# Performance work log

Hardware: AMD Instinct MI355X
Metric: run time of the kernel (lower is better)

## Reference

```python
import jax, jax.numpy as jnp
import numpy as np

N = 8192
IN_F = 256
OUT_F = 128
ALPHA = 0.2
NEG = -9000000000000000.0

def setup_inputs() -> dict:
    key = jax.random.key(0)
    k1, k2, k3, k4 = jax.random.split(key, 4)
    h = jax.random.normal(k1, (N, IN_F), dtype=jnp.float32)
    adj = jax.random.randint(k2, (N, N), 0, 2, dtype=jnp.int32)
    # xavier-uniform-like params
    limW = float(np.sqrt(6.0 / (IN_F + OUT_F)))
    W = jax.random.uniform(k3, (IN_F, OUT_F), minval=-limW, maxval=limW, dtype=jnp.float32)
    lima = float(np.sqrt(6.0 / (2 * OUT_F + 1)))
    a = jax.random.uniform(k4, (2 * OUT_F, 1), minval=-lima, maxval=lima, dtype=jnp.float32)
    return {"h": h, "adj": adj, "W": W, "a": a}

def reference(h, adj, W, a):
    Wh = h @ W  # [N, F]
    # e_ij = LeakyReLU(a1.Wh_i + a2.Wh_j) -- avoids [N,N,2F] intermediate
    a1 = a[:OUT_F, 0]  # [F]
    a2 = a[OUT_F:, 0]  # [F]
    f1 = Wh @ a1  # [N]
    f2 = Wh @ a2  # [N]
    e = jax.nn.leaky_relu(f1[:, None] + f2[None, :], negative_slope=ALPHA)  # [N,N]
    att = jnp.where(adj > 0, e, jnp.float32(NEG))
    att = jax.nn.softmax(att, axis=1)
    h_prime = att @ Wh  # [N, F]
    return h_prime
```

## Files before the change

kernel.cpp:

```cpp
#include <hip/hip_runtime.h>
#include <hip/hip_bf16.h>

#define N    8192
#define INF  256
#define OUTF 128
#define ALPHA 0.2f

typedef __attribute__((ext_vector_type(8))) short bf16x8;
typedef __attribute__((ext_vector_type(4))) float f32x4;

__device__ __forceinline__ unsigned short f2bf(float x) {
    union { float f; unsigned u; } v; v.f = x;
    unsigned r = v.u + 0x7fff + ((v.u >> 16) & 1);
    return (unsigned short)(r >> 16);
}
__device__ __forceinline__ float bf2f(unsigned short b) {
    union { unsigned u; float f; } v; v.u = ((unsigned)b) << 16;
    return v.f;
}

__global__ __launch_bounds__(256) void k1_wh(
        const float* __restrict__ h, const float* __restrict__ W,
        const float* __restrict__ a,
        unsigned short* __restrict__ WhTb, float* __restrict__ f1, float* __restrict__ f2) {
    __shared__ float hs[8][INF];
    const int t  = threadIdx.x;
    const int i0 = blockIdx.x * 8;

    #pragma unroll
    for (int u = 0; u < 2; ++u) {
        int idx = u * 256 + t;
        int r   = idx >> 6;
        int kq  = idx & 63;
        *(float4*)&hs[r][kq * 4] = *(const float4*)(h + (size_t)(i0 + r) * INF + kq * 4);
    }
    __syncthreads();

    const int rg = t >> 5;
    const int ct = t & 31;
    float acc[4] = {0.f, 0.f, 0.f, 0.f};

    #pragma unroll 8
    for (int k = 0; k < INF; ++k) {
        float4 wv = *(const float4*)(W + (size_t)k * OUTF + ct * 4);
        float  hx = hs[rg][k];
        acc[0] += hx * wv.x; acc[1] += hx * wv.y;
        acc[2] += hx * wv.z; acc[3] += hx * wv.w;
    }

    const int r0 = i0 + rg;
    const int jb = r0 >> 5;
    const int jo = r0 & 31;
    #pragma unroll
    for (int cc = 0; cc < 4; ++cc)
        WhTb[(size_t)jb * 4096 + (ct * 4 + cc) * 32 + jo] = f2bf(acc[cc]);

    const float4 a1v = *(const float4*)(a + ct * 4);
    const float4 a2v = *(const float4*)(a + OUTF + ct * 4);
    float p1 = acc[0]*a1v.x + acc[1]*a1v.y + acc[2]*a1v.z + acc[3]*a1v.w;
    float p2 = acc[0]*a2v.x + acc[1]*a2v.y + acc[2]*a2v.z + acc[3]*a2v.w;
    #pragma unroll
    for (int off = 16; off > 0; off >>= 1) {
        p1 += __shfl_down(p1, off, 32);
        p2 += __shfl_down(p2, off, 32);
    }
    if (ct == 0) { f1[r0] = p1; f2[r0] = p2; }
}

struct PF { int4 a0, a1; float4 g0, g1; };

__device__ __forceinline__ PF ldpf(const int* __restrict__ ap,
                                   const float* __restrict__ gp, int jt) {
    PF p;
    p.a0 = *(const int4*)  (ap + (size_t)jt * 32);
    p.a1 = *(const int4*)  (ap + (size_t)jt * 32 + 4);
    p.g0 = *(const float4*)(gp + (size_t)jt * 32);
    p.g1 = *(const float4*)(gp + (size_t)jt * 32 + 4);
    return p;
}

#define EXP1(AV, FV, IDX)                                                   \
    {                                                                       \
        float s_ = f1r + (FV);                                              \
        float e_ = s_ > 0.f ? s_ : ALPHA * s_;                              \
        float p_ = ((AV) > 0) ? __expf(e_) : 0.f;                           \
        unsigned short pb_ = f2bf(p_);                                      \
        afrag[IDX] = (short)pb_;                                            \
        dsum += bf2f(pb_);                                                  \
    }

#define K2ITER(PFV, JT)                                                     \
    {                                                                       \
        const unsigned short* wp_ = WhTb + ((size_t)(w * 32 + (JT))) * 4096 + laneb; \
        bf16x8 b0_ = *(const bf16x8*)(wp_);                                 \
        bf16x8 b1_ = *(const bf16x8*)(wp_ + 512);                           \
        bf16x8 b2_ = *(const bf16x8*)(wp_ + 1024);                          \
        bf16x8 b3_ = *(const bf16x8*)(wp_ + 1536);                          \
        bf16x8 b4_ = *(const bf16x8*)(wp_ + 2048);                          \
        bf16x8 b5_ = *(const bf16x8*)(wp_ + 2560);                          \
        bf16x8 b6_ = *(const bf16x8*)(wp_ + 3072);                          \
        bf16x8 b7_ = *(const bf16x8*)(wp_ + 3584);                          \
        int4 A0_ = PFV.a0, A1_ = PFV.a1;                                    \
        float4 F0_ = PFV.g0, F1_ = PFV.g1;                                  \
        if ((JT) + 2 < NT) PFV = ldpf(adjp, f2p, (JT) + 2);                 \
        bf16x8 afrag;                                                       \
        EXP1(A0_.x, F0_.x, 0) EXP1(A0_.y, F0_.y, 1)                         \
        EXP1(A0_.z, F0_.z, 2) EXP1(A0_.w, F0_.w, 3)                         \
        EXP1(A1_.x, F1_.x, 4) EXP1(A1_.y, F1_.y, 5)                         \
        EXP1(A1_.z, F1_.z, 6) EXP1(A1_.w, F1_.w, 7)                         \
        acc0 = __builtin_amdgcn_mfma_f32_16x16x32_bf16(afrag, b0_, acc0, 0, 0, 0); \
        acc1 = __builtin_amdgcn_mfma_f32_16x16x32_bf16(afrag, b1_, acc1, 0, 0, 0); \
        acc2 = __builtin_amdgcn_mfma_f32_16x16x32_bf16(afrag, b2_, acc2, 0, 0, 0); \
        acc3 = __builtin_amdgcn_mfma_f32_16x16x32_bf16(afrag, b3_, acc3, 0, 0, 0); \
        acc4 = __builtin_amdgcn_mfma_f32_16x16x32_bf16(afrag, b4_, acc4, 0, 0, 0); \
        acc5 = __builtin_amdgcn_mfma_f32_16x16x32_bf16(afrag, b5_, acc5, 0, 0, 0); \
        acc6 = __builtin_amdgcn_mfma_f32_16x16x32_bf16(afrag, b6_, acc6, 0, 0, 0); \
        acc7 = __builtin_amdgcn_mfma_f32_16x16x32_bf16(afrag, b7_, acc7, 0, 0, 0); \
    }

__global__ __launch_bounds__(512, 4) void k2_attn(
        const int* __restrict__ adj, const unsigned short* __restrict__ WhTb,
        const float* __restrict__ f1, const float* __restrict__ f2,
        float* __restrict__ out) {
    __shared__ float red[8][16][132];
    __shared__ float den_s[8][16];

    const int t    = threadIdx.x;
    const int w    = t >> 6;
    const int ln   = t & 63;
    const int m16  = ln & 15;
    const int quad = ln >> 4;
    const int i0   = blockIdx.x * 16;
    const int row  = i0 + m16;

    const float f1r = f1[row];
    const int   j0w = w * (N / 8);
    const int   NT  = (N / 8) / 32;

    const int*   adjp  = adj + (size_t)row * N + j0w + quad * 8;
    const float* f2p   = f2 + j0w + quad * 8;
    const int    laneb = m16 * 32 + quad * 8;

    f32x4 acc0 = {0.f,0.f,0.f,0.f}, acc1 = {0.f,0.f,0.f,0.f};
    f32x4 acc2 = {0.f,0.f,0.f,0.f}, acc3 = {0.f,0.f,0.f,0.f};
    f32x4 acc4 = {0.f,0.f,0.f,0.f}, acc5 = {0.f,0.f,0.f,0.f};
    f32x4 acc6 = {0.f,0.f,0.f,0.f}, acc7 = {0.f,0.f,0.f,0.f};
    float dsum = 0.f;

    PF pf0 = ldpf(adjp, f2p, 0);
    PF pf1 = ldpf(adjp, f2p, 1);

    for (int jt = 0; jt < NT; jt += 2) {
        K2ITER(pf0, jt)
        K2ITER(pf1, jt + 1)
    }

    dsum += __shfl_xor(dsum, 16);
    dsum += __shfl_xor(dsum, 32);
    if (quad == 0) den_s[w][m16] = dsum;

    #pragma unroll
    for (int r = 0; r < 4; ++r) {
        red[w][quad * 4 + r][0 * 16 + m16] = acc0[r];
        red[w][quad * 4 + r][1 * 16 + m16] = acc1[r];
        red[w][quad * 4 + r][2 * 16 + m16] = acc2[r];
        red[w][quad * 4 + r][3 * 16 + m16] = acc3[r];
        red[w][quad * 4 + r][4 * 16 + m16] = acc4[r];
        red[w][quad * 4 + r][5 * 16 + m16] = acc5[r];
        red[w][quad * 4 + r][6 * 16 + m16] = acc6[r];
        red[w][quad * 4 + r][7 * 16 + m16] = acc7[r];
    }
    __syncthreads();

    {
        int r  = t >> 5;
        int c4 = (t & 31) * 4;
        float4 sv = {0.f,0.f,0.f,0.f};
        float dtot = 0.f;
        #pragma unroll
        for (int ww = 0; ww < 8; ++ww) {
            float4 v = *(const float4*)&red[ww][r][c4];
            sv.x += v.x; sv.y += v.y; sv.z += v.z; sv.w += v.w;
            dtot += den_s[ww][r];
        }
        const float inv = 1.0f / dtot;
        float4 o = {sv.x * inv, sv.y * inv, sv.z * inv, sv.w * inv};
        *(float4*)(out + (size_t)(i0 + r) * OUTF + c4) = o;
    }
}

extern "C" void kernel_launch(void* const* d_in, const int* in_sizes, int n_in,
                              void* d_out, int out_size, void* d_ws, size_t ws_size,
                              hipStream_t stream) {
    const float* h   = (const float*)d_in[0];
    const int*   adj = (const int*)  d_in[1];
    const float* W   = (const float*)d_in[2];
    const float* a   = (const float*)d_in[3];
    float* out = (float*)d_out;

    unsigned short* WhTb = (unsigned short*)d_ws;
    float* f1 = (float*)(WhTb + (size_t)N * OUTF);
    float* f2 = f1 + N;

    k1_wh  <<<N / 8, 256, 0, stream>>>(h, W, a, WhTb, f1, f2);
    k2_attn<<<N / 16, 512, 0, stream>>>(adj, WhTb, f1, f2, out);
}
```

Before: 527.9 us.

## Split attention K-range over 4 waves and load f2 on demand

Reduces the attention kernel block from 8 waves to 4, so each wave covers twice as many columns and the cross-wave shared-memory reduction is half the size. Only the adjacency ints stay in the two-deep register prefetch; f2 values are now loaded inline in each step, which cuts register pressure. Launch bounds change from (512,4) to (256,3). The adj read stays the dominant traffic, so the main risks are fewer waves in flight to hide HBM latency and exposed f2 load latency.

```diff
diff --git a/kernel.cpp b/kernel.cpp
--- a/kernel.cpp
+++ b/kernel.cpp
@@ -67,15 +67,12 @@
     if (ct == 0) { f1[r0] = p1; f2[r0] = p2; }
 }
 
-struct PF { int4 a0, a1; float4 g0, g1; };
-
-__device__ __forceinline__ PF ldpf(const int* __restrict__ ap,
-                                   const float* __restrict__ gp, int jt) {
-    PF p;
-    p.a0 = *(const int4*)  (ap + (size_t)jt * 32);
-    p.a1 = *(const int4*)  (ap + (size_t)jt * 32 + 4);
-    p.g0 = *(const float4*)(gp + (size_t)jt * 32);
-    p.g1 = *(const float4*)(gp + (size_t)jt * 32 + 4);
+struct PFA { int4 a0, a1; };
+
+__device__ __forceinline__ PFA ldadj(const int* __restrict__ ap, int jt) {
+    PFA p;
+    p.a0 = *(const int4*)(ap + (size_t)jt * 32);
+    p.a1 = *(const int4*)(ap + (size_t)jt * 32 + 4);
     return p;
 }
 
@@ -89,9 +86,9 @@
         dsum += bf2f(pb_);                                                  \
     }
 
-#define K2ITER(PFV, JT)                                                     \
+#define K2STEP(PFV, JT)                                                     \
     {                                                                       \
-        const unsigned short* wp_ = WhTb + ((size_t)(w * 32 + (JT))) * 4096 + laneb; \
+        const unsigned short* wp_ = WhTb + ((size_t)(w * 64 + (JT))) * 4096 + laneb; \
         bf16x8 b0_ = *(const bf16x8*)(wp_);                                 \
         bf16x8 b1_ = *(const bf16x8*)(wp_ + 512);                           \
         bf16x8 b2_ = *(const bf16x8*)(wp_ + 1024);                          \
@@ -100,9 +97,10 @@
         bf16x8 b5_ = *(const bf16x8*)(wp_ + 2560);                          \
         bf16x8 b6_ = *(const bf16x8*)(wp_ + 3072);                          \
         bf16x8 b7_ = *(const bf16x8*)(wp_ + 3584);                          \
+        float4 F0_ = *(const float4*)(f2p + (size_t)(JT) * 32);             \
+        float4 F1_ = *(const float4*)(f2p + (size_t)(JT) * 32 + 4);         \
         int4 A0_ = PFV.a0, A1_ = PFV.a1;                                    \
-        float4 F0_ = PFV.g0, F1_ = PFV.g1;                                  \
-        if ((JT) + 2 < NT) PFV = ldpf(adjp, f2p, (JT) + 2);                 \
+        if ((JT) + 2 < NT) PFV = ldadj(adjp, (JT) + 2);                     \
         bf16x8 afrag;                                                       \
         EXP1(A0_.x, F0_.x, 0) EXP1(A0_.y, F0_.y, 1)                         \
         EXP1(A0_.z, F0_.z, 2) EXP1(A0_.w, F0_.w, 3)                         \
@@ -118,12 +116,12 @@
         acc7 = __builtin_amdgcn_mfma_f32_16x16x32_bf16(afrag, b7_, acc7, 0, 0, 0); \
     }
 
-__global__ __launch_bounds__(512, 4) void k2_attn(
+__global__ __launch_bounds__(256, 3) void k2_attn(
         const int* __restrict__ adj, const unsigned short* __restrict__ WhTb,
         const float* __restrict__ f1, const float* __restrict__ f2,
         float* __restrict__ out) {
-    __shared__ float red[8][16][132];
-    __shared__ float den_s[8][16];
+    __shared__ float red[4][16][132];
+    __shared__ float den_s[4][16];
 
     const int t    = threadIdx.x;
     const int w    = t >> 6;
@@ -134,8 +132,8 @@
     const int row  = i0 + m16;
 
     const float f1r = f1[row];
-    const int   j0w = w * (N / 8);
-    const int   NT  = (N / 8) / 32;
+    const int   j0w = w * (N / 4);
+    const int   NT  = (N / 4) / 32;
 
     const int*   adjp  = adj + (size_t)row * N + j0w + quad * 8;
     const float* f2p   = f2 + j0w + quad * 8;
@@ -147,12 +145,12 @@
     f32x4 acc6 = {0.f,0.f,0.f,0.f}, acc7 = {0.f,0.f,0.f,0.f};
     float dsum = 0.f;
 
-    PF pf0 = ldpf(adjp, f2p, 0);
-    PF pf1 = ldpf(adjp, f2p, 1);
+    PFA pf0 = ldadj(adjp, 0);
+    PFA pf1 = ldadj(adjp, 1);
 
     for (int jt = 0; jt < NT; jt += 2) {
-        K2ITER(pf0, jt)
-        K2ITER(pf1, jt + 1)
+        K2STEP(pf0, jt)
+        K2STEP(pf1, jt + 1)
     }
 
     dsum += __shfl_xor(dsum, 16);
@@ -172,19 +170,22 @@
     }
     __syncthreads();
 
-    {
-        int r  = t >> 5;
-        int c4 = (t & 31) * 4;
-        float4 sv = {0.f,0.f,0.f,0.f};
-        float dtot = 0.f;
-        #pragma unroll
-        for (int ww = 0; ww < 8; ++ww) {
-            float4 v = *(const float4*)&red[ww][r][c4];
-            sv.x += v.x; sv.y += v.y; sv.z += v.z; sv.w += v.w;
-            dtot += den_s[ww][r];
-        }
-        const float inv = 1.0f / dtot;
-        float4 o = {sv.x * inv, sv.y * inv, sv.z * inv, sv.w * inv};
+    #pragma unroll
+    for (int e = 0; e < 2; ++e) {
+        int idx = e * 256 + t;
+        int r   = idx >> 5;
+        int c4  = (idx & 31) * 4;
+        float4 s0 = *(const float4*)&red[0][r][c4];
+        float4 s1 = *(const float4*)&red[1][r][c4];
+        float4 s2 = *(const float4*)&red[2][r][c4];
+        float4 s3 = *(const float4*)&red[3][r][c4];
+        float dtot = den_s[0][r] + den_s[1][r] + den_s[2][r] + den_s[3][r];
+        float inv  = 1.0f / dtot;
+        float4 o;
+        o.x = (s0.x + s1.x + s2.x + s3.x) * inv;
+        o.y = (s0.y + s1.y + s2.y + s3.y) * inv;
+        o.z = (s0.z + s1.z + s2.z + s3.z) * inv;
+        o.w = (s0.w + s1.w + s2.w + s3.w) * inv;
         *(float4*)(out + (size_t)(i0 + r) * OUTF + c4) = o;
     }
 }
@@ -203,5 +204,5 @@
     float* f2 = f1 + N;
 
     k1_wh  <<<N / 8, 256, 0, stream>>>(h, W, a, WhTb, f1, f2);
-    k2_attn<<<N / 16, 512, 0, stream>>>(adj, WhTb, f1, f2, out);
-}
+    k2_attn<<<N / 16, 256, 0, stream>>>(adj, WhTb, f1, f2, out);
+}
```

Result: faster. 452.3 us (-14.3%).
